# Kernel tuning notes

Measured on AMD Instinct MI355X. Metric: run time of the kernel, lower is better.

## Reference

```python
import jax, jax.numpy as jnp
import numpy as np

GLM_HIDDEN = 256
K = 3
REL_NUM = K + 1
NUM_BASES = 2
BATCH = 8
SLEN = 2048


def setup_inputs() -> dict:
    key = jax.random.key(0)
    k1, k2, k3, k4, k5 = jax.random.split(key, 5)
    D = GLM_HIDDEN
    x = jax.random.normal(k1, (BATCH, SLEN, D), dtype=jnp.float32)
    # RGCNConv basis decomposition params: W_r = sum_b comp[r,b] * basis[b]
    scale = 1.0 / np.sqrt(D)
    basis = jax.random.normal(k2, (NUM_BASES, D, D), dtype=jnp.float32) * scale
    comp = jax.random.normal(k3, (REL_NUM, NUM_BASES), dtype=jnp.float32)
    root = jax.random.normal(k4, (D, D), dtype=jnp.float32) * scale
    bias = jax.random.normal(k5, (D,), dtype=jnp.float32) * 0.01
    return {"x": x, "comp": comp, "basis": basis, "root": root, "bias": bias}


def reference(x, comp, basis, root, bias):
    B, S, D = x.shape
    R = comp.shape[0]
    Kthr = R - 1
    idx = jnp.arange(S)
    # edge (source s -> target t) has relation min(|t+1 - s|, K); full S x S edge set
    rel = jnp.minimum(jnp.abs((idx[None, :] + 1) - idx[:, None]), Kthr)  # [S(source), S(target)]
    masks = (rel[None, :, :] == jnp.arange(R)[:, None, None]).astype(x.dtype)  # [R,S,T]
    deg = masks.sum(axis=1)  # [R,T] in-degree per relation (PyG aggr='mean')
    inv_deg = jnp.where(deg > 0, 1.0 / deg, 0.0)
    A = masks * inv_deg[:, None, :]  # normalized adjacency per relation [R,S,T]
    # basis-decomposed relation weights
    W = jnp.einsum('rb,bio->rio', comp, basis)  # [R,D,D]
    # aggregate then transform: out[b,t] = sum_r (mean_{s in N_r(t)} x[b,s]) @ W_r
    agg = jnp.einsum('rst,bsi->brti', A, x)  # [B,R,S,D]
    out = jnp.einsum('brti,rio->bto', agg, W)
    out = out + jnp.einsum('bsi,io->bso', x, root) + bias
    return out
```

## Files before the change

### kernel.cpp

```cpp
#include <hip/hip_runtime.h>

#define D 256
#define S 2048
#define B 8
#define DSQ (D * D)
#define INV3 (1.0f / 2043.0f)

typedef __bf16 bf16x8 __attribute__((ext_vector_type(8)));
typedef float f32x4 __attribute__((ext_vector_type(4)));

__device__ __forceinline__ unsigned short f2bf(float f) {
    union { float f; unsigned int u; } v; v.f = f;
    unsigned int u = v.u;
    u += 0x7fffu + ((u >> 16) & 1u);
    return (unsigned short)(u >> 16);
}

__device__ __forceinline__ void gl2lds16(const void* g, void* l) {
    __builtin_amdgcn_global_load_lds(
        (const __attribute__((address_space(1))) void*)g,
        (__attribute__((address_space(3))) void*)l, 16, 0, 0);
}

__global__ __launch_bounds__(256) void k_prep(const float* __restrict__ x,
                                              const float* __restrict__ comp,
                                              const float* __restrict__ basis,
                                              const float* __restrict__ root,
                                              unsigned short* __restrict__ xh,
                                              float* __restrict__ tot,
                                              unsigned short* __restrict__ Cbs) {
    int blk = blockIdx.x;
    int tid = threadIdx.x;
    int b = blk >> 6, chunk = blk & 63;
    __shared__ float ps[4][D];
    int rg = tid >> 6;
    int c4 = (tid & 63) << 2;
    int row0 = chunk * 32 + rg * 8;
    const float4* xb = (const float4*)(x + ((size_t)b * S + row0) * D + c4);
    ushort4* dst = (ushort4*)(xh + ((size_t)(1 + b * S + row0)) * D + c4);
    float4 s = {0.f, 0.f, 0.f, 0.f};
    #pragma unroll
    for (int i = 0; i < 8; ++i) {
        float4 v = xb[(size_t)i * 64];
        ushort4 o;
        o.x = f2bf(v.x); o.y = f2bf(v.y); o.z = f2bf(v.z); o.w = f2bf(v.w);
        dst[(size_t)i * 64] = o;
        s.x += v.x; s.y += v.y; s.z += v.z; s.w += v.w;
    }
    *(float4*)&ps[rg][c4] = s;

    if (blk < 192) {
        int step = blk >> 2, q = blk & 3;
        int ji = step >> 3, kc = step & 7;
        int n = tid;
        float a0 = (ji == 2) ? 1.f : 0.f;
        float a1 = (ji == 1 || ji == 3) ? 0.5f : 0.f;
        float a2 = (ji == 0 || ji == 4) ? 0.5f : 0.f;
        float ar = (ji == 1) ? 1.f : 0.f;
        float s3 = (ji == 5) ? INV3 : -INV3;
        float cb0 = a0 * comp[0] + a1 * comp[2] + a2 * comp[4] + s3 * comp[6];
        float cb1 = a0 * comp[1] + a1 * comp[3] + a2 * comp[5] + s3 * comp[7];
        unsigned short buf[8];
        #pragma unroll
        for (int kk = 0; kk < 8; ++kk) {
            int i = kc * 32 + q * 8 + kk;
            buf[kk] = f2bf(cb0 * basis[i * D + n] + cb1 * basis[DSQ + i * D + n]
                           + ar * root[i * D + n]);
        }
        *(uint4*)(Cbs + ((size_t)step * 256 + n) * 32 + q * 8) = *(uint4*)buf;
    }
    __syncthreads();
    float v = ps[0][tid] + ps[1][tid] + ps[2][tid] + ps[3][tid];
    atomicAdd(tot + b * D + tid, v);
}

__global__ __launch_bounds__(256, 2) void k_bulk(
        const unsigned short* __restrict__ xh,
        const unsigned short* __restrict__ Cbs,
        const float* __restrict__ tot,
        const float* __restrict__ basis, const float* __restrict__ root,
        const float* __restrict__ bias, const float* __restrict__ comp,
        const float* __restrict__ x, float* __restrict__ out) {
    __shared__ __align__(16) unsigned short xs[68 * 256];
    __shared__ __align__(16) unsigned short tot_s[256];
    const int tid = threadIdx.x;
    const int blk = blockIdx.x;

    if (blk < 32) {
        const int q3 = blk & 3, b2 = blk >> 2;
        const int t = (q3 == 0) ? 0 : (S - 4 + q3);
        float* z0 = (float*)xs; float* z1 = z0 + D; float* xr = z0 + 2 * D;
        const float* xb2 = x + (size_t)b2 * S * D;
        const int i = tid;
        float tt = tot[b2 * D + i];
        float x_t = xb2[(size_t)t * D + i];
        float v0 = (t + 1 < S) ? xb2[(size_t)(t + 1) * D + i] : 0.f;
        float d1 = 1.f + ((t + 2 < S) ? 1.f : 0.f);
        float v1 = (x_t + ((t + 2 < S) ? xb2[(size_t)(t + 2) * D + i] : 0.f)) / d1;
        float s2 = ((t - 1 >= 0) ? xb2[(size_t)(t - 1) * D + i] : 0.f)
                 + ((t + 3 < S) ? xb2[(size_t)(t + 3) * D + i] : 0.f);
        int d2i = ((t - 1 >= 0) ? 1 : 0) + ((t + 3 < S) ? 1 : 0);
        float v2 = d2i ? s2 / (float)d2i : 0.f;
        float wsum = 0.f;
        for (int ss = t - 1; ss <= t + 3; ++ss)
            if (ss >= 0 && ss < S) wsum += xb2[(size_t)ss * D + i];
        int d3i = ((t - 1 > 0) ? (t - 1) : 0) + ((S - 4 - t > 0) ? (S - 4 - t) : 0);
        float v3 = d3i ? (tt - wsum) / (float)d3i : 0.f;
        z0[i] = comp[0] * v0 + comp[2] * v1 + comp[4] * v2 + comp[6] * v3;
        z1[i] = comp[1] * v0 + comp[3] * v1 + comp[5] * v2 + comp[7] * v3;
        xr[i] = x_t;
        __syncthreads();
        int o = tid;
        float a2c = 0.f;
        #pragma unroll 8
        for (int k = 0; k < D; ++k)
            a2c += z0[k] * basis[k * D + o] + z1[k] * basis[DSQ + k * D + o]
                 + xr[k] * root[k * D + o];
        out[(((size_t)b2 * S + t) << 8) + o] = a2c + bias[o];
        return;
    }

    const int g    = blk - 32;
    const int lane = tid & 63;
    const int w    = tid >> 6;
    const int nblk = g & 1;
    const int mblk = g >> 1;
    const int bq   = mblk >> 5;
    const int t0   = (mblk & 31) << 6;
    const size_t rowbase = (size_t)bq * S + t0;

    #pragma unroll
    for (int q = 0; q < 8; ++q) {
        int F = (q * 256 + tid) * 16;
        int r = F >> 9;
        int c16 = (F >> 4) & 31;
        int gc = (c16 & 24) | ((c16 ^ r) & 7);
        gl2lds16((const char*)xh + ((rowbase + r) << 9) + (gc << 4), (char*)xs + F);
    }
    if (tid < 128) {
        int F = (2048 + tid) * 16;
        int r = F >> 9;
        int c16 = (F >> 4) & 31;
        int gc = (c16 & 24) | ((c16 ^ r) & 7);
        gl2lds16((const char*)xh + ((rowbase + r) << 9) + (gc << 4), (char*)xs + F);
    }
    if (tid < 64) {
        float4 tv = *(const float4*)(tot + bq * D + tid * 4);
        ushort4 o;
        o.x = f2bf(tv.x); o.y = f2bf(tv.y); o.z = f2bf(tv.z); o.w = f2bf(tv.w);
        *(ushort4*)(tot_s + tid * 4) = o;
    }
    __syncthreads();

    const int rlo = lane & 15, q4 = lane >> 4;
    const int nstrip = nblk * 128 + w * 32;

    #define BFRAG(st, nt) (*(const bf16x8*)(Cbs + \
        (((size_t)(st) * 256 + nstrip + (nt) * 16 + rlo) << 5) + (q4 << 3)))
    #define AFRAG(st, mt) (*(const bf16x8*)((const char*)xs + \
        ((((mt) * 16 + rlo + ((st) >> 3))) << 9) + \
        (((((st) & 7) * 4 + q4) & 24 | ((((st) & 7) * 4 + q4) ^ \
          ((mt) * 16 + rlo + ((st) >> 3))) & 7) << 4)))
    #define AVFRAG(kc) (*(const bf16x8*)((const char*)tot_s + ((kc) << 6) + (q4 << 4)))

    f32x4 acc[4][2] = {};
    bf16x8 bb[4][2];
    bf16x8 aa[2][4];
    #pragma unroll
    for (int nt = 0; nt < 2; ++nt) {
        bb[0][nt] = BFRAG(0, nt); bb[1][nt] = BFRAG(1, nt); bb[2][nt] = BFRAG(2, nt);
    }
    #pragma unroll
    for (int mt = 0; mt < 4; ++mt) aa[0][mt] = AFRAG(0, mt);

    #define MFMA8(s) \
        acc[0][0] = __builtin_amdgcn_mfma_f32_16x16x32_bf16(aa[(s)&1][0], bb[(s)&3][0], acc[0][0], 0, 0, 0); \
        acc[0][1] = __builtin_amdgcn_mfma_f32_16x16x32_bf16(aa[(s)&1][0], bb[(s)&3][1], acc[0][1], 0, 0, 0); \
        acc[1][0] = __builtin_amdgcn_mfma_f32_16x16x32_bf16(aa[(s)&1][1], bb[(s)&3][0], acc[1][0], 0, 0, 0); \
        acc[1][1] = __builtin_amdgcn_mfma_f32_16x16x32_bf16(aa[(s)&1][1], bb[(s)&3][1], acc[1][1], 0, 0, 0); \
        acc[2][0] = __builtin_amdgcn_mfma_f32_16x16x32_bf16(aa[(s)&1][2], bb[(s)&3][0], acc[2][0], 0, 0, 0); \
        acc[2][1] = __builtin_amdgcn_mfma_f32_16x16x32_bf16(aa[(s)&1][2], bb[(s)&3][1], acc[2][1], 0, 0, 0); \
        acc[3][0] = __builtin_amdgcn_mfma_f32_16x16x32_bf16(aa[(s)&1][3], bb[(s)&3][0], acc[3][0], 0, 0, 0); \
        acc[3][1] = __builtin_amdgcn_mfma_f32_16x16x32_bf16(aa[(s)&1][3], bb[(s)&3][1], acc[3][1], 0, 0, 0);

    #define KSTEP(s) { \
        bb[((s)+3)&3][0] = BFRAG((((s)+3) < 48) ? ((s)+3) : 47, 0); \
        bb[((s)+3)&3][1] = BFRAG((((s)+3) < 48) ? ((s)+3) : 47, 1); \
        if (((s)+1) < 40) { \
            aa[((s)+1)&1][0] = AFRAG(((s)+1) & 63, 0); \
            aa[((s)+1)&1][1] = AFRAG(((s)+1) & 63, 1); \
            aa[((s)+1)&1][2] = AFRAG(((s)+1) & 63, 2); \
            aa[((s)+1)&1][3] = AFRAG(((s)+1) & 63, 3); \
        } else { \
            bf16x8 av_ = AVFRAG((((s)+1) - 40) & 7); \
            aa[((s)+1)&1][0] = av_; aa[((s)+1)&1][1] = av_; \
            aa[((s)+1)&1][2] = av_; aa[((s)+1)&1][3] = av_; \
        } \
        MFMA8(s) }

    KSTEP(0)  KSTEP(1)  KSTEP(2)  KSTEP(3)  KSTEP(4)  KSTEP(5)  KSTEP(6)  KSTEP(7)
    KSTEP(8)  KSTEP(9)  KSTEP(10) KSTEP(11) KSTEP(12) KSTEP(13) KSTEP(14) KSTEP(15)
    KSTEP(16) KSTEP(17) KSTEP(18) KSTEP(19) KSTEP(20) KSTEP(21) KSTEP(22) KSTEP(23)
    KSTEP(24) KSTEP(25) KSTEP(26) KSTEP(27) KSTEP(28) KSTEP(29) KSTEP(30) KSTEP(31)
    KSTEP(32) KSTEP(33) KSTEP(34) KSTEP(35) KSTEP(36) KSTEP(37) KSTEP(38) KSTEP(39)
    KSTEP(40) KSTEP(41) KSTEP(42) KSTEP(43) KSTEP(44) KSTEP(45) KSTEP(46) KSTEP(47)

    #undef KSTEP
    #undef MFMA8
    #undef BFRAG
    #undef AFRAG
    #undef AVFRAG

    const int col = lane & 15, rq = (lane >> 4) << 2;
    #pragma unroll
    for (int nt = 0; nt < 2; ++nt) {
        int n = nstrip + nt * 16 + col;
        float bi = bias[n];
        #pragma unroll
        for (int mt = 0; mt < 4; ++mt) {
            #pragma unroll
            for (int i = 0; i < 4; ++i) {
                int t = t0 + mt * 16 + rq + i;
                if (t >= 1 && t <= S - 4)
                    out[(((size_t)bq * S + t) << 8) + n] = acc[mt][nt][i] + bi;
            }
        }
    }
}


extern "C" void kernel_launch(void* const* d_in, const int* in_sizes, int n_in,
                              void* d_out, int out_size, void* d_ws, size_t ws_size,
                              hipStream_t stream) {
    const float* x     = (const float*)d_in[0];
    const float* comp  = (const float*)d_in[1];
    const float* basis = (const float*)d_in[2];
    const float* root  = (const float*)d_in[3];
    const float* bias  = (const float*)d_in[4];
    float* out = (float*)d_out;

    char* ws = (char*)d_ws;
    float* tot          = (float*)(ws);
    unsigned short* Cbs = (unsigned short*)(ws + 8192);
    unsigned short* xh  = (unsigned short*)(ws + 794624);

    hipMemsetAsync(tot, 0, B * D * sizeof(float), stream);
    k_prep<<<512, 256, 0, stream>>>(x, comp, basis, root, xh, tot, Cbs);
    k_bulk<<<544, 256, 0, stream>>>(xh, Cbs, tot, basis, root, bias, comp, x, out);
}
```

Baseline: 101.8 us.

## Replace atomic column-sum with per-block partials and split mean-term MFMAs

Drops the memset launch and the atomicAdd reduction: each prep block writes its column partial sums, and every bulk block re-reduces 64 partials for its batch. The column-mean term now goes into a separate 2-tile accumulator instead of broadcasting it into all four M-tiles, which cuts the last eight K-steps from eight MFMAs to two. In exchange every bulk block does 64 extra strided global loads per thread, and the workspace grows.

```diff
diff --git a/kernel.cpp b/kernel.cpp
--- a/kernel.cpp
+++ b/kernel.cpp
@@ -27,7 +27,7 @@
                                               const float* __restrict__ basis,
                                               const float* __restrict__ root,
                                               unsigned short* __restrict__ xh,
-                                              float* __restrict__ tot,
+                                              float* __restrict__ part,
                                               unsigned short* __restrict__ Cbs) {
     int blk = blockIdx.x;
     int tid = threadIdx.x;
@@ -70,14 +70,16 @@
         *(uint4*)(Cbs + ((size_t)step * 256 + n) * 32 + q * 8) = *(uint4*)buf;
     }
     __syncthreads();
-    float v = ps[0][tid] + ps[1][tid] + ps[2][tid] + ps[3][tid];
-    atomicAdd(tot + b * D + tid, v);
+    if (tid < 64)
+        *(float4*)&part[(size_t)blk * D + tid * 4] =
+            *(float4*)&ps[0][tid * 4] + *(float4*)&ps[1][tid * 4] +
+            *(float4*)&ps[2][tid * 4] + *(float4*)&ps[3][tid * 4];
 }
 
 __global__ __launch_bounds__(256, 2) void k_bulk(
         const unsigned short* __restrict__ xh,
         const unsigned short* __restrict__ Cbs,
-        const float* __restrict__ tot,
+        const float* __restrict__ part,
         const float* __restrict__ basis, const float* __restrict__ root,
         const float* __restrict__ bias, const float* __restrict__ comp,
         const float* __restrict__ x, float* __restrict__ out) {
@@ -92,7 +94,9 @@
         float* z0 = (float*)xs; float* z1 = z0 + D; float* xr = z0 + 2 * D;
         const float* xb2 = x + (size_t)b2 * S * D;
         const int i = tid;
-        float tt = tot[b2 * D + i];
+        float tt = 0.f;
+        #pragma unroll 8
+        for (int c = 0; c < 64; ++c) tt += part[(size_t)(b2 * 64 + c) * D + i];
         float x_t = xb2[(size_t)t * D + i];
         float v0 = (t + 1 < S) ? xb2[(size_t)(t + 1) * D + i] : 0.f;
         float d1 = 1.f + ((t + 2 < S) ? 1.f : 0.f);
@@ -144,11 +148,11 @@
         int gc = (c16 & 24) | ((c16 ^ r) & 7);
         gl2lds16((const char*)xh + ((rowbase + r) << 9) + (gc << 4), (char*)xs + F);
     }
-    if (tid < 64) {
-        float4 tv = *(const float4*)(tot + bq * D + tid * 4);
-        ushort4 o;
-        o.x = f2bf(tv.x); o.y = f2bf(tv.y); o.z = f2bf(tv.z); o.w = f2bf(tv.w);
-        *(ushort4*)(tot_s + tid * 4) = o;
+    {
+        float t = 0.f;
+        #pragma unroll 8
+        for (int c = 0; c < 64; ++c) t += part[(size_t)(bq * 64 + c) * D + tid];
+        tot_s[tid] = f2bf(t);
     }
     __syncthreads();
 
@@ -164,6 +168,7 @@
     #define AVFRAG(kc) (*(const bf16x8*)((const char*)tot_s + ((kc) << 6) + (q4 << 4)))
 
     f32x4 acc[4][2] = {};
+    f32x4 accT[2] = {};
     bf16x8 bb[4][2];
     bf16x8 aa[2][4];
     #pragma unroll
@@ -187,24 +192,28 @@
         bb[((s)+3)&3][0] = BFRAG((((s)+3) < 48) ? ((s)+3) : 47, 0); \
         bb[((s)+3)&3][1] = BFRAG((((s)+3) < 48) ? ((s)+3) : 47, 1); \
         if (((s)+1) < 40) { \
-            aa[((s)+1)&1][0] = AFRAG(((s)+1) & 63, 0); \
-            aa[((s)+1)&1][1] = AFRAG(((s)+1) & 63, 1); \
-            aa[((s)+1)&1][2] = AFRAG(((s)+1) & 63, 2); \
-            aa[((s)+1)&1][3] = AFRAG(((s)+1) & 63, 3); \
-        } else { \
-            bf16x8 av_ = AVFRAG((((s)+1) - 40) & 7); \
-            aa[((s)+1)&1][0] = av_; aa[((s)+1)&1][1] = av_; \
-            aa[((s)+1)&1][2] = av_; aa[((s)+1)&1][3] = av_; \
+            aa[((s)+1)&1][0] = AFRAG((((s)+1) < 40) ? ((s)+1) : 39, 0); \
+            aa[((s)+1)&1][1] = AFRAG((((s)+1) < 40) ? ((s)+1) : 39, 1); \
+            aa[((s)+1)&1][2] = AFRAG((((s)+1) < 40) ? ((s)+1) : 39, 2); \
+            aa[((s)+1)&1][3] = AFRAG((((s)+1) < 40) ? ((s)+1) : 39, 3); \
         } \
         MFMA8(s) }
+
+    #define TSTEP(s) { \
+        bb[((s)+3)&3][0] = BFRAG((((s)+3) < 48) ? ((s)+3) : 47, 0); \
+        bb[((s)+3)&3][1] = BFRAG((((s)+3) < 48) ? ((s)+3) : 47, 1); \
+        bf16x8 av_ = AVFRAG((s) - 40); \
+        accT[0] = __builtin_amdgcn_mfma_f32_16x16x32_bf16(av_, bb[(s)&3][0], accT[0], 0, 0, 0); \
+        accT[1] = __builtin_amdgcn_mfma_f32_16x16x32_bf16(av_, bb[(s)&3][1], accT[1], 0, 0, 0); }
 
     KSTEP(0)  KSTEP(1)  KSTEP(2)  KSTEP(3)  KSTEP(4)  KSTEP(5)  KSTEP(6)  KSTEP(7)
     KSTEP(8)  KSTEP(9)  KSTEP(10) KSTEP(11) KSTEP(12) KSTEP(13) KSTEP(14) KSTEP(15)
     KSTEP(16) KSTEP(17) KSTEP(18) KSTEP(19) KSTEP(20) KSTEP(21) KSTEP(22) KSTEP(23)
     KSTEP(24) KSTEP(25) KSTEP(26) KSTEP(27) KSTEP(28) KSTEP(29) KSTEP(30) KSTEP(31)
     KSTEP(32) KSTEP(33) KSTEP(34) KSTEP(35) KSTEP(36) KSTEP(37) KSTEP(38) KSTEP(39)
-    KSTEP(40) KSTEP(41) KSTEP(42) KSTEP(43) KSTEP(44) KSTEP(45) KSTEP(46) KSTEP(47)
-
+    TSTEP(40) TSTEP(41) TSTEP(42) TSTEP(43) TSTEP(44) TSTEP(45) TSTEP(46) TSTEP(47)
+
+    #undef TSTEP
     #undef KSTEP
     #undef MFMA8
     #undef BFRAG
@@ -222,7 +231,8 @@
             for (int i = 0; i < 4; ++i) {
                 int t = t0 + mt * 16 + rq + i;
                 if (t >= 1 && t <= S - 4)
-                    out[(((size_t)bq * S + t) << 8) + n] = acc[mt][nt][i] + bi;
+                    out[(((size_t)bq * S + t) << 8) + n] =
+                        acc[mt][nt][i] + accT[nt][i] + bi;
             }
         }
     }
@@ -240,11 +250,10 @@
     float* out = (float*)d_out;
 
     char* ws = (char*)d_ws;
-    float* tot          = (float*)(ws);
-    unsigned short* Cbs = (unsigned short*)(ws + 8192);
-    unsigned short* xh  = (unsigned short*)(ws + 794624);
-
-    hipMemsetAsync(tot, 0, B * D * sizeof(float), stream);
-    k_prep<<<512, 256, 0, stream>>>(x, comp, basis, root, xh, tot, Cbs);
-    k_bulk<<<544, 256, 0, stream>>>(xh, Cbs, tot, basis, root, bias, comp, x, out);
-}
+    float* part         = (float*)(ws);
+    unsigned short* Cbs = (unsigned short*)(ws + 524288);
+    unsigned short* xh  = (unsigned short*)(ws + 1310720);
+
+    k_prep<<<512, 256, 0, stream>>>(x, comp, basis, root, xh, part, Cbs);
+    k_bulk<<<544, 256, 0, stream>>>(xh, Cbs, part, basis, root, bias, comp, x, out);
+}
```

After: 102.9 us. Within noise of the previous version (+1.1%).
